# Kernel tuning notes

Measured on AMD Instinct MI355X. Metric: run time of the kernel, lower is better.

## Reference

```python
import jax, jax.numpy as jnp
import numpy as np

MAX_ABS = 1.0          # assumed get_max_abs('T')
DT = 0.01              # forward default dt
TWO_PI = 2.0 * np.pi
B, D, N = 4096, 2048, 4096


def setup_inputs() -> dict:
    key = jax.random.key(0)
    k0, k1 = jax.random.split(key, 2)
    x = jax.random.normal(k0, (B, D), dtype=jnp.float32)
    # nn.Linear params
    W = jax.random.normal(k1, (N, D), dtype=jnp.float32) * (1.0 / np.sqrt(D))
    b = jnp.zeros((N,), dtype=jnp.float32)
    # oscillator params (as initialized in __init__)
    amplitude = jnp.ones((N,), dtype=jnp.float32)
    frequency = jnp.ones((N,), dtype=jnp.float32)
    phase_offset = jnp.zeros((N,), dtype=jnp.float32)
    damping = jnp.full((N,), 0.01, dtype=jnp.float32)
    return {"x": x, "W": W, "b": b, "amplitude": amplitude,
            "frequency": frequency, "phase_offset": phase_offset,
            "damping": damping}


def reference(x, W, b, amplitude, frequency, phase_offset, damping):
    # driving force: [B, N]
    force = x @ W.T + b
    omega_sq = (TWO_PI * frequency) ** 2  # [N]
    # t starts at 0 and is incremented ONCE per forward call
    t = DT

    def step(carry, f):
        state, vel = carry
        accel = -omega_sq * state - damping * vel + f
        vel = vel + accel * DT
        state = state + vel * DT
        return (state, vel), state

    init = (jnp.zeros((N,), x.dtype), jnp.zeros((N,), x.dtype))
    (_, _), states = jax.lax.scan(step, init, force)  # states: [B, N]

    # sinusoid term is identical for every batch step (t fixed within forward)
    osc = amplitude * jnp.sin(TWO_PI * frequency * t + phase_offset)  # [N]
    out = jnp.clip(states + osc, -MAX_ABS, MAX_ABS)
    return out
```

## Files before the change

### kernel.cpp

```cpp
#include <hip/hip_runtime.h>
#include <hip/hip_bf16.h>
#include <math.h>

#define MDIM 4096
#define KDIM 2048
#define NDIM 4096
#define DT   0.01f
#define TWO_PI_F 6.283185307179586f
#define CH 64
#define CL 64

typedef __attribute__((ext_vector_type(8))) short bf16x8;
typedef __attribute__((ext_vector_type(4))) float f32x4;

#define GLD_LDS16(g, l)                                             \
  __builtin_amdgcn_global_load_lds(                                 \
      (const __attribute__((address_space(1))) unsigned int*)(g),   \
      (__attribute__((address_space(3))) unsigned int*)(l), 16, 0, 0)

__device__ __forceinline__ unsigned short f2bf(float f) {
  unsigned int u = __float_as_uint(f);
  u += 0x7FFFu + ((u >> 16) & 1u);
  return (unsigned short)(u >> 16);
}
__device__ __forceinline__ float bf2f(unsigned short u) {
  return __uint_as_float(((unsigned int)u) << 16);
}

__global__ void cast2_bf16_kernel(const float* __restrict__ s0,
                                  unsigned short* __restrict__ d0,
                                  const float* __restrict__ s1,
                                  unsigned short* __restrict__ d1,
                                  int n4each) {
  int i = blockIdx.x * blockDim.x + threadIdx.x;
  const float4* sp;
  ushort4* dp;
  int j;
  if (i < n4each) { sp = (const float4*)s0; dp = (ushort4*)d0; j = i; }
  else            { sp = (const float4*)s1; dp = (ushort4*)d1; j = i - n4each; }
  float4 v = sp[j];
  ushort4 o;
  o.x = f2bf(v.x); o.y = f2bf(v.y); o.z = f2bf(v.z); o.w = f2bf(v.w);
  dp[j] = o;
}

__global__ __launch_bounds__(256, 2) void gemm_bt_kernel(
    const unsigned short* __restrict__ A,
    const unsigned short* __restrict__ Bm,
    const float* __restrict__ bias,
    unsigned short* __restrict__ C) {
  __shared__ __align__(16) unsigned short sA[128 * 32];
  __shared__ __align__(16) unsigned short sB[128 * 32];

  const int tid  = threadIdx.x;
  const int lane = tid & 63;
  const int wave = tid >> 6;
  const int wr = wave >> 1;
  const int wc = wave & 1;
  const int q  = lane >> 4;
  const int lm = lane & 15;

  const int bM = blockIdx.x * 128;
  const int bN = blockIdx.y * 128;

  f32x4 acc[4][4];
#pragma unroll
  for (int i = 0; i < 4; i++)
#pragma unroll
    for (int j = 0; j < 4; j++) acc[i][j] = (f32x4){0.f, 0.f, 0.f, 0.f};

  const int idx0 = tid;
  const int idx1 = tid + 256;
  const int r0 = idx0 >> 2, c0 = (idx0 & 3) * 8;
  const int r1 = idx1 >> 2, c1 = (idx1 & 3) * 8;
  const unsigned short* gA0 = A  + (size_t)(bM + r0) * KDIM + c0;
  const unsigned short* gA1 = A  + (size_t)(bM + r1) * KDIM + c1;
  const unsigned short* gB0 = Bm + (size_t)(bN + r0) * KDIM + c0;
  const unsigned short* gB1 = Bm + (size_t)(bN + r1) * KDIM + c1;

  for (int k0 = 0; k0 < KDIM; k0 += 32) {
    __syncthreads();
    GLD_LDS16(gA0 + k0, &sA[idx0 * 8]);
    GLD_LDS16(gA1 + k0, &sA[idx1 * 8]);
    GLD_LDS16(gB0 + k0, &sB[idx0 * 8]);
    GLD_LDS16(gB1 + k0, &sB[idx1 * 8]);
    __syncthreads();

    bf16x8 af[4], bfr[4];
#pragma unroll
    for (int mt = 0; mt < 4; mt++)
      af[mt]  = *(const bf16x8*)&sA[(wr * 64 + mt * 16 + lm) * 32 + q * 8];
#pragma unroll
    for (int nt = 0; nt < 4; nt++)
      bfr[nt] = *(const bf16x8*)&sB[(wc * 64 + nt * 16 + lm) * 32 + q * 8];

#pragma unroll
    for (int mt = 0; mt < 4; mt++)
#pragma unroll
      for (int nt = 0; nt < 4; nt++)
        acc[mt][nt] = __builtin_amdgcn_mfma_f32_16x16x32_bf16(
            af[mt], bfr[nt], acc[mt][nt], 0, 0, 0);
  }

#pragma unroll
  for (int nt = 0; nt < 4; nt++) {
    const int col = bN + wc * 64 + nt * 16 + lm;
    const float bz = bias[col];
#pragma unroll
    for (int mt = 0; mt < 4; mt++) {
      const int row0 = bM + wr * 64 + mt * 16 + q * 4;
#pragma unroll
      for (int r = 0; r < 4; r++)
        C[(size_t)(row0 + r) * NDIM + col] = f2bf(acc[mt][nt][r] + bz);
    }
  }
}

__global__ void scan_pass1(const unsigned short* __restrict__ force,
                           const float* __restrict__ freq,
                           const float* __restrict__ damp,
                           float* __restrict__ chunkS,
                           float* __restrict__ chunkV) {
  int gid = blockIdx.x * blockDim.x + threadIdx.x;
  int n4 = gid & (NDIM / 4 - 1);
  int c  = gid >> 10;
  int n  = n4 * 4;
  float4 fr = *(const float4*)&freq[n];
  float4 dv = *(const float4*)&damp[n];
  float osq[4] = {TWO_PI_F * fr.x, TWO_PI_F * fr.y, TWO_PI_F * fr.z, TWO_PI_F * fr.w};
  float dp[4]  = {dv.x, dv.y, dv.z, dv.w};
  float s[4] = {0.f, 0.f, 0.f, 0.f}, v[4] = {0.f, 0.f, 0.f, 0.f};
#pragma unroll
  for (int j = 0; j < 4; j++) osq[j] *= osq[j];
  const unsigned short* fp = force + (size_t)c * CL * NDIM + n;
#pragma unroll 4
  for (int i = 0; i < CL; i++) {
    ushort4 fv = *(const ushort4*)&fp[(size_t)i * NDIM];
    float f[4] = {bf2f(fv.x), bf2f(fv.y), bf2f(fv.z), bf2f(fv.w)};
#pragma unroll
    for (int j = 0; j < 4; j++) {
      float a = -osq[j] * s[j] - dp[j] * v[j] + f[j];
      v[j] += a * DT;
      s[j] += v[j] * DT;
    }
  }
  *(float4*)&chunkS[c * NDIM + n] = (float4){s[0], s[1], s[2], s[3]};
  *(float4*)&chunkV[c * NDIM + n] = (float4){v[0], v[1], v[2], v[3]};
}

__global__ void scan_pass2(const float* __restrict__ chunkS,
                           const float* __restrict__ chunkV,
                           const float* __restrict__ freq,
                           const float* __restrict__ damp,
                           float* __restrict__ carryS,
                           float* __restrict__ carryV) {
  int n = blockIdx.x * blockDim.x + threadIdx.x;
  float om = TWO_PI_F * freq[n];
  float osq = om * om;
  float dp = damp[n];
  float a00 = 1.f - osq * DT * DT, a01 = DT * (1.f - dp * DT);
  float a10 = -osq * DT,           a11 = 1.f - dp * DT;
#pragma unroll
  for (int i = 0; i < 6; i++) {
    float b00 = a00 * a00 + a01 * a10;
    float b01 = a00 * a01 + a01 * a11;
    float b10 = a10 * a00 + a11 * a10;
    float b11 = a10 * a01 + a11 * a11;
    a00 = b00; a01 = b01; a10 = b10; a11 = b11;
  }
  float cs = 0.f, cv = 0.f;
#pragma unroll 8
  for (int c = 0; c < CH; c++) {
    carryS[c * NDIM + n] = cs;
    carryV[c * NDIM + n] = cv;
    float ls = chunkS[c * NDIM + n];
    float lv = chunkV[c * NDIM + n];
    float ns = a00 * cs + a01 * cv + ls;
    float nv = a10 * cs + a11 * cv + lv;
    cs = ns; cv = nv;
  }
}

__global__ void scan_pass3(const unsigned short* __restrict__ force,
                           const float* __restrict__ amp,
                           const float* __restrict__ freq,
                           const float* __restrict__ phase,
                           const float* __restrict__ damp,
                           const float* __restrict__ carryS,
                           const float* __restrict__ carryV,
                           float* __restrict__ out) {
  int gid = blockIdx.x * blockDim.x + threadIdx.x;
  int n4 = gid & (NDIM / 4 - 1);
  int c  = gid >> 10;
  int n  = n4 * 4;
  float4 fr = *(const float4*)&freq[n];
  float4 dv = *(const float4*)&damp[n];
  float4 am = *(const float4*)&amp[n];
  float4 ph = *(const float4*)&phase[n];
  float om[4] = {TWO_PI_F * fr.x, TWO_PI_F * fr.y, TWO_PI_F * fr.z, TWO_PI_F * fr.w};
  float dp[4] = {dv.x, dv.y, dv.z, dv.w};
  float osq[4], osc[4], s[4], v[4];
  float amv[4] = {am.x, am.y, am.z, am.w};
  float phv[4] = {ph.x, ph.y, ph.z, ph.w};
#pragma unroll
  for (int j = 0; j < 4; j++) {
    osq[j] = om[j] * om[j];
    osc[j] = amv[j] * sinf(om[j] * DT + phv[j]);
  }
  float4 csv = *(const float4*)&carryS[c * NDIM + n];
  float4 cvv = *(const float4*)&carryV[c * NDIM + n];
  s[0] = csv.x; s[1] = csv.y; s[2] = csv.z; s[3] = csv.w;
  v[0] = cvv.x; v[1] = cvv.y; v[2] = cvv.z; v[3] = cvv.w;
  const unsigned short* fp = force + (size_t)c * CL * NDIM + n;
  float* op = out + (size_t)c * CL * NDIM + n;
#pragma unroll 4
  for (int i = 0; i < CL; i++) {
    ushort4 fv = *(const ushort4*)&fp[(size_t)i * NDIM];
    float f[4] = {bf2f(fv.x), bf2f(fv.y), bf2f(fv.z), bf2f(fv.w)};
    float o[4];
#pragma unroll
    for (int j = 0; j < 4; j++) {
      float a = -osq[j] * s[j] - dp[j] * v[j] + f[j];
      v[j] += a * DT;
      s[j] += v[j] * DT;
      o[j] = fminf(1.f, fmaxf(-1.f, s[j] + osc[j]));
    }
    *(float4*)&op[(size_t)i * NDIM] = (float4){o[0], o[1], o[2], o[3]};
  }
}

extern "C" void kernel_launch(void* const* d_in, const int* in_sizes, int n_in,
                              void* d_out, int out_size, void* d_ws, size_t ws_size,
                              hipStream_t stream) {
  const float* x     = (const float*)d_in[0];
  const float* W     = (const float*)d_in[1];
  const float* bias  = (const float*)d_in[2];
  const float* amp   = (const float*)d_in[3];
  const float* freq  = (const float*)d_in[4];
  const float* phase = (const float*)d_in[5];
  const float* damp  = (const float*)d_in[6];

  unsigned short* xbf   = (unsigned short*)d_ws;
  unsigned short* wbf   = xbf + (size_t)MDIM * KDIM;
  unsigned short* force = wbf + (size_t)NDIM * KDIM;
  float* chunkS = (float*)d_ws;
  float* chunkV = chunkS + CH * NDIM;
  float* carryS = chunkV + CH * NDIM;
  float* carryV = carryS + CH * NDIM;

  const int n4each = MDIM * KDIM / 4;
  cast2_bf16_kernel<<<(2 * n4each + 255) / 256, 256, 0, stream>>>(
      x, xbf, W, wbf, n4each);

  dim3 gg(MDIM / 128, NDIM / 128);
  gemm_bt_kernel<<<gg, 256, 0, stream>>>(xbf, wbf, bias, force);

  scan_pass1<<<CH * NDIM / 4 / 256, 256, 0, stream>>>(force, freq, damp,
                                                      chunkS, chunkV);
  scan_pass2<<<NDIM / 256, 256, 0, stream>>>(chunkS, chunkV, freq, damp,
                                             carryS, carryV);
  scan_pass3<<<CH * NDIM / 4 / 256, 256, 0, stream>>>(
      force, amp, freq, phase, damp, carryS, carryV, (float*)d_out);
}
```

Measured before the change: 231.4 us.

## Use register-staged global loads with XOR-swizzled LDS and K-tile of 64

The GEMM main loop now loads tiles into registers with plain vector global loads, then writes them to LDS using an XOR swizzle, replacing the direct global-to-LDS loads. The K tile doubles from 32 to 64, which halves the number of barrier pairs per K sweep and runs two MFMA sub-steps per tile. The swizzle is meant to remove LDS bank conflicts on the fragment reads. The cost is more registers and twice the LDS per block, and global loads are still not overlapped with compute because there is only a single buffer.

```diff
diff --git a/kernel.cpp b/kernel.cpp
--- a/kernel.cpp
+++ b/kernel.cpp
@@ -12,11 +12,6 @@
 
 typedef __attribute__((ext_vector_type(8))) short bf16x8;
 typedef __attribute__((ext_vector_type(4))) float f32x4;
-
-#define GLD_LDS16(g, l)                                             \
-  __builtin_amdgcn_global_load_lds(                                 \
-      (const __attribute__((address_space(1))) unsigned int*)(g),   \
-      (__attribute__((address_space(3))) unsigned int*)(l), 16, 0, 0)
 
 __device__ __forceinline__ unsigned short f2bf(float f) {
   unsigned int u = __float_as_uint(f);
@@ -49,8 +44,9 @@
     const unsigned short* __restrict__ Bm,
     const float* __restrict__ bias,
     unsigned short* __restrict__ C) {
-  __shared__ __align__(16) unsigned short sA[128 * 32];
-  __shared__ __align__(16) unsigned short sB[128 * 32];
+  __shared__ __align__(16) unsigned short smem[16384];
+  unsigned short* sA = smem;
+  unsigned short* sB = smem + 8192;
 
   const int tid  = threadIdx.x;
   const int lane = tid & 63;
@@ -69,37 +65,59 @@
 #pragma unroll
     for (int j = 0; j < 4; j++) acc[i][j] = (f32x4){0.f, 0.f, 0.f, 0.f};
 
-  const int idx0 = tid;
-  const int idx1 = tid + 256;
-  const int r0 = idx0 >> 2, c0 = (idx0 & 3) * 8;
-  const int r1 = idx1 >> 2, c1 = (idx1 & 3) * 8;
-  const unsigned short* gA0 = A  + (size_t)(bM + r0) * KDIM + c0;
-  const unsigned short* gA1 = A  + (size_t)(bM + r1) * KDIM + c1;
-  const unsigned short* gB0 = Bm + (size_t)(bN + r0) * KDIM + c0;
-  const unsigned short* gB1 = Bm + (size_t)(bN + r1) * KDIM + c1;
-
-  for (int k0 = 0; k0 < KDIM; k0 += 32) {
+  const unsigned short* gA[4];
+  const unsigned short* gB[4];
+  int dst[4];
+#pragma unroll
+  for (int p = 0; p < 4; p++) {
+    int slot = tid + 256 * p;
+    int row  = slot >> 3;
+    int g    = slot & 7;
+    gA[p] = A  + (size_t)(bM + row) * KDIM + g * 8;
+    gB[p] = Bm + (size_t)(bN + row) * KDIM + g * 8;
+    dst[p] = row * 64 + ((g ^ (row & 7)) * 8);
+  }
+
+  int roA[4], roB[4];
+#pragma unroll
+  for (int t = 0; t < 4; t++) {
+    roA[t] = (wr * 64 + t * 16 + lm) * 64;
+    roB[t] = (wc * 64 + t * 16 + lm) * 64;
+  }
+  const int swz = lm & 7;
+
+  for (int k0 = 0; k0 < KDIM; k0 += 64) {
+    uint4 av[4], bv[4];
+#pragma unroll
+    for (int p = 0; p < 4; p++) {
+      av[p] = *(const uint4*)(gA[p] + k0);
+      bv[p] = *(const uint4*)(gB[p] + k0);
+    }
     __syncthreads();
-    GLD_LDS16(gA0 + k0, &sA[idx0 * 8]);
-    GLD_LDS16(gA1 + k0, &sA[idx1 * 8]);
-    GLD_LDS16(gB0 + k0, &sB[idx0 * 8]);
-    GLD_LDS16(gB1 + k0, &sB[idx1 * 8]);
+#pragma unroll
+    for (int p = 0; p < 4; p++) {
+      *(uint4*)&sA[dst[p]] = av[p];
+      *(uint4*)&sB[dst[p]] = bv[p];
+    }
     __syncthreads();
 
-    bf16x8 af[4], bfr[4];
-#pragma unroll
-    for (int mt = 0; mt < 4; mt++)
-      af[mt]  = *(const bf16x8*)&sA[(wr * 64 + mt * 16 + lm) * 32 + q * 8];
-#pragma unroll
-    for (int nt = 0; nt < 4; nt++)
-      bfr[nt] = *(const bf16x8*)&sB[(wc * 64 + nt * 16 + lm) * 32 + q * 8];
-
-#pragma unroll
-    for (int mt = 0; mt < 4; mt++)
+#pragma unroll
+    for (int kk = 0; kk < 2; kk++) {
+      bf16x8 af[4], bfr[4];
+#pragma unroll
+      for (int mt = 0; mt < 4; mt++)
+        af[mt]  = *(const bf16x8*)&sA[roA[mt] + (((kk * 4 + q) ^ swz) * 8)];
 #pragma unroll
       for (int nt = 0; nt < 4; nt++)
-        acc[mt][nt] = __builtin_amdgcn_mfma_f32_16x16x32_bf16(
-            af[mt], bfr[nt], acc[mt][nt], 0, 0, 0);
+        bfr[nt] = *(const bf16x8*)&sB[roB[nt] + (((kk * 4 + q) ^ swz) * 8)];
+
+#pragma unroll
+      for (int mt = 0; mt < 4; mt++)
+#pragma unroll
+        for (int nt = 0; nt < 4; nt++)
+          acc[mt][nt] = __builtin_amdgcn_mfma_f32_16x16x32_bf16(
+              af[mt], bfr[nt], acc[mt][nt], 0, 0, 0);
+    }
   }
 
 #pragma unroll
```

Result: slower. 450.5 us (+94.7%).
